# Performance work log

Measured on AMD Instinct MI355X. Metric: run time of the kernel, lower is better.

The kernel has to match this reference:

```python
import jax, jax.numpy as jnp
import numpy as np

B, S, D, H, L, NS = 16, 1024, 512, 8, 4, 4
HD = D // H            # head dim = 64
FF = 4 * D             # dim_feedforward
VOCAB = 64
OUT = 64


def _ln(x, g, b, eps=1e-5):
    m = jnp.mean(x, -1, keepdims=True)
    v = jnp.var(x, -1, keepdims=True)
    return (x - m) * jax.lax.rsqrt(v + eps) * g + b


def setup_inputs() -> dict:
    key = jax.random.key(0)
    ks = iter(jax.random.split(key, 40))
    def w(shape, s=0.02):
        return jax.random.normal(next(ks), shape, jnp.float32) * s
    return {
        "x_batch": jax.random.randint(next(ks), (B, S), 0, VOCAB),
        "context_batch": jax.random.normal(next(ks), (B, 2), jnp.float32),
        "specialist_ids": jax.random.randint(next(ks), (B,), 0, NS),
        "emb_table": w((VOCAB, D), 1.0),
        "wqkv": w((L, D, 3 * D)), "bqkv": jnp.zeros((L, 3 * D), jnp.float32),
        "wo": w((L, D, D)), "bo": jnp.zeros((L, D), jnp.float32),
        "ln1_g": jnp.ones((L, D), jnp.float32), "ln1_b": jnp.zeros((L, D), jnp.float32),
        "w1": w((L, D, FF)), "b1": jnp.zeros((L, FF), jnp.float32),
        "w2": w((L, FF, D)), "b2": jnp.zeros((L, D), jnp.float32),
        "ln2_g": jnp.ones((L, D), jnp.float32), "ln2_b": jnp.zeros((L, D), jnp.float32),
        "ctx_w": w((2, D)), "ctx_b": jnp.zeros((D,), jnp.float32),
        "ca_wq": w((D, D)), "ca_bq": jnp.zeros((D,), jnp.float32),
        "ca_wk": w((D, D)), "ca_bk": jnp.zeros((D,), jnp.float32),
        "ca_wv": w((D, D)), "ca_bv": jnp.zeros((D,), jnp.float32),
        "ca_wo": w((D, D)), "ca_bo": jnp.zeros((D,), jnp.float32),
        "pred_w": w((NS, D, OUT)), "pred_b": jnp.zeros((NS, OUT), jnp.float32),
        "act_w": w((NS, D, OUT)), "act_b": jnp.zeros((NS, OUT), jnp.float32),
    }


def _forward(x_batch, context_batch, specialist_ids, emb_table,
             wqkv, bqkv, wo, bo, ln1_g, ln1_b, w1, b1, w2, b2, ln2_g, ln2_b,
             ctx_w, ctx_b, ca_wq, ca_bq, ca_wk, ca_bk, ca_wv, ca_bv, ca_wo, ca_bo,
             pred_w, pred_b, act_w, act_b):
    b, s = x_batch.shape
    x = emb_table[x_batch]                                   # [B,S,D]
    causal = jnp.triu(jnp.full((s, s), -jnp.inf, jnp.float32), 1)
    scale = 1.0 / np.sqrt(HD)
    nlayers = wqkv.shape[0]
    for i in range(nlayers):  # post-LN TransformerEncoderLayer (torch default)
        qkv = x @ wqkv[i] + bqkv[i]
        q, k, v = jnp.split(qkv, 3, axis=-1)
        q = q.reshape(b, s, H, HD)
        k = k.reshape(b, s, H, HD)
        v = v.reshape(b, s, H, HD)
        scores = jnp.einsum('bqhd,bkhd->bhqk', q, k) * scale + causal
        a = jax.nn.softmax(scores, axis=-1)
        o = jnp.einsum('bhqk,bkhd->bqhd', a, v).reshape(b, s, -1)
        x = _ln(x + o @ wo[i] + bo[i], ln1_g[i], ln1_b[i])
        ff = jax.nn.relu(x @ w1[i] + b1[i]) @ w2[i] + b2[i]
        x = _ln(x + ff, ln2_g[i], ln2_b[i])
    # single-token cross attention: kv comes from projected context
    ctx = (context_batch @ ctx_w + ctx_b)[:, None, :]        # [B,1,D]
    q = (x @ ca_wq + ca_bq).reshape(b, s, H, HD)
    k = (ctx @ ca_wk + ca_bk).reshape(b, 1, H, HD)
    v = (ctx @ ca_wv + ca_bv).reshape(b, 1, H, HD)
    sc = jnp.einsum('bqhd,bkhd->bhqk', q, k) * scale         # [B,H,S,1]
    a = jax.nn.softmax(sc, axis=-1)                          # all ones (kv_len=1)
    o = jnp.einsum('bhqk,bkhd->bqhd', a, v).reshape(b, s, -1)
    latent = o @ ca_wo + ca_bo                               # no residual, as in source
    last = latent[:, -1, :]                                  # [B,D]
    # specialist dispatch: gather per-sample expert weights, batched GEMV
    pred = jnp.einsum('bd,bdo->bo', last, pred_w[specialist_ids]) + pred_b[specialist_ids]
    act = jnp.einsum('bd,bdo->bo', last, act_w[specialist_ids]) + act_b[specialist_ids]
    return pred, act


def reference(x_batch, context_batch, specialist_ids, emb_table,
              wqkv, bqkv, wo, bo, ln1_g, ln1_b, w1, b1, w2, b2, ln2_g, ln2_b,
              ctx_w, ctx_b, ca_wq, ca_bq, ca_wk, ca_bk, ca_wv, ca_bv, ca_wo, ca_bo,
              pred_w, pred_b, act_w, act_b):
    return _forward(x_batch, context_batch, specialist_ids, emb_table,
                    wqkv, bqkv, wo, bo, ln1_g, ln1_b, w1, b1, w2, b2, ln2_g, ln2_b,
                    ctx_w, ctx_b, ca_wq, ca_bq, ca_wk, ca_bk, ca_wv, ca_bv, ca_wo, ca_bo,
                    pred_w, pred_b, act_w, act_b)
```

## Files before the change

kernel.cpp:

```cpp
#include <hip/hip_runtime.h>
#include <hip/hip_bf16.h>


#define DD 512
#define BB 16
#define OO 64
#define NC 8

__global__ __launch_bounds__(256) void k1_v(
    const float* __restrict__ cb, const float* __restrict__ cw,
    const float* __restrict__ cbias, const float* __restrict__ wv,
    float* __restrict__ vpart) {
  __shared__ float cs[BB * 64];
  __shared__ float red[4 * BB * 64];
  const int tid = threadIdx.x;
  const int jb = blockIdx.x & 7, db = blockIdx.x >> 3;
  const int d0 = db * 64, j0 = jb * 64;

  for (int idx = tid; idx < BB * 64; idx += 256) {
    const int b = idx >> 6, d = idx & 63;
    cs[idx] = fmaf(cb[2 * b], cw[d0 + d],
               fmaf(cb[2 * b + 1], cw[DD + d0 + d], cbias[d0 + d]));
  }
  __syncthreads();

  const int j = tid & 63, dsub = tid >> 6;
  float acc[BB];
#pragma unroll
  for (int b = 0; b < BB; ++b) acc[b] = 0.f;
  float wr[16];
#pragma unroll
  for (int i = 0; i < 16; ++i)
    wr[i] = wv[(d0 + dsub * 16 + i) * DD + j0 + j];
#pragma unroll
  for (int i = 0; i < 16; ++i) {
    const int d = dsub * 16 + i;
#pragma unroll
    for (int b = 0; b < BB; ++b) acc[b] = fmaf(cs[b * 64 + d], wr[i], acc[b]);
  }
#pragma unroll
  for (int b = 0; b < BB; ++b) red[dsub * (BB * 64) + b * 64 + j] = acc[b];
  __syncthreads();
  for (int idx = tid; idx < BB * 64; idx += 256) {
    float s = red[idx] + red[idx + BB * 64] + red[idx + 2 * BB * 64] + red[idx + 3 * BB * 64];
    const int b = idx >> 6, jj = idx & 63;
    vpart[(db * BB + b) * DD + j0 + jj] = s;
  }
}

__global__ __launch_bounds__(256) void k2_o(
    const float* __restrict__ bv, const float* __restrict__ wo,
    const float* __restrict__ vpart, float* __restrict__ lpart) {
  __shared__ float vs[BB * 64];
  __shared__ float red[4 * BB * 64];
  const int tid = threadIdx.x;
  const int jb = blockIdx.x & 7, db = blockIdx.x >> 3;
  const int d0 = db * 64, j0 = jb * 64;

  for (int idx = tid; idx < BB * 64; idx += 256) {
    const int b = idx >> 6, d = idx & 63;
    float s = bv[d0 + d];
#pragma unroll
    for (int c = 0; c < NC; ++c) s += vpart[(c * BB + b) * DD + d0 + d];
    vs[idx] = s;
  }
  __syncthreads();

  const int j = tid & 63, dsub = tid >> 6;
  float acc[BB];
#pragma unroll
  for (int b = 0; b < BB; ++b) acc[b] = 0.f;
  float wr[16];
#pragma unroll
  for (int i = 0; i < 16; ++i)
    wr[i] = wo[(d0 + dsub * 16 + i) * DD + j0 + j];
#pragma unroll
  for (int i = 0; i < 16; ++i) {
    const int d = dsub * 16 + i;
#pragma unroll
    for (int b = 0; b < BB; ++b) acc[b] = fmaf(vs[b * 64 + d], wr[i], acc[b]);
  }
#pragma unroll
  for (int b = 0; b < BB; ++b) red[dsub * (BB * 64) + b * 64 + j] = acc[b];
  __syncthreads();
  for (int idx = tid; idx < BB * 64; idx += 256) {
    float s = red[idx] + red[idx + BB * 64] + red[idx + 2 * BB * 64] + red[idx + 3 * BB * 64];
    const int b = idx >> 6, jj = idx & 63;
    lpart[(db * BB + b) * DD + j0 + jj] = s;
  }
}

__global__ __launch_bounds__(512) void k3_head(
    const float* __restrict__ bo, const float* __restrict__ lpart,
    const int* __restrict__ sid,
    const float* __restrict__ pw, const float* __restrict__ pb,
    const float* __restrict__ aw, const float* __restrict__ ab,
    float* __restrict__ out) {
  __shared__ float ls[DD];
  __shared__ float red[8 * OO];
  const int tid = threadIdx.x;
  const int b = blockIdx.x & 15, half = blockIdx.x >> 4;

  for (int d = tid; d < DD; d += 512) {
    float s = bo[d];
#pragma unroll
    for (int c = 0; c < NC; ++c) s += lpart[(c * BB + b) * DD + d];
    ls[d] = s;
  }
  __syncthreads();

  const int s = sid[b];
  const int o = tid & 63, dsub = tid >> 6;
  const float* w = (half ? aw : pw) + (s * DD + dsub * 64) * OO + o;
  float acc = 0.f;
#pragma unroll 16
  for (int i = 0; i < 64; ++i)
    acc = fmaf(ls[dsub * 64 + i], w[i * OO], acc);
  red[dsub * OO + o] = acc;
  __syncthreads();
  if (tid < OO) {
    float a = (half ? ab : pb)[s * OO + tid];
#pragma unroll
    for (int p = 0; p < 8; ++p) a += red[p * OO + tid];
    out[half * (BB * OO) + b * OO + tid] = a;
  }
}

extern "C" void kernel_launch(void* const* d_in, const int* in_sizes, int n_in,
                              void* d_out, int out_size, void* d_ws, size_t ws_size,
                              hipStream_t stream) {
  const float* cb    = reinterpret_cast<const float*>(d_in[1]);
  const int*   sid   = reinterpret_cast<const int*>(d_in[2]);
  const float* cw    = reinterpret_cast<const float*>(d_in[16]);
  const float* cbias = reinterpret_cast<const float*>(d_in[17]);
  const float* wv    = reinterpret_cast<const float*>(d_in[22]);
  const float* bv    = reinterpret_cast<const float*>(d_in[23]);
  const float* wo    = reinterpret_cast<const float*>(d_in[24]);
  const float* bo    = reinterpret_cast<const float*>(d_in[25]);
  const float* pw    = reinterpret_cast<const float*>(d_in[26]);
  const float* pb    = reinterpret_cast<const float*>(d_in[27]);
  const float* aw    = reinterpret_cast<const float*>(d_in[28]);
  const float* ab    = reinterpret_cast<const float*>(d_in[29]);

  float* vpart = reinterpret_cast<float*>(d_ws);
  float* lpart = vpart + NC * BB * DD;

  k1_v   <<<64, 256, 0, stream>>>(cb, cw, cbias, wv, vpart);
  k2_o   <<<64, 256, 0, stream>>>(bv, wo, vpart, lpart);
  k3_head<<<32, 512, 0, stream>>>(bo, lpart, sid, pw, pb, aw, ab,
                                  reinterpret_cast<float*>(d_out));
}
```

Measured before the change: 144.6 us.

## Exploit linearity in context to propagate three basis vectors instead of batch

```diff
diff --git a/kernel.cpp b/kernel.cpp
--- a/kernel.cpp
+++ b/kernel.cpp
@@ -1,5 +1,4 @@
 #include <hip/hip_runtime.h>
-#include <hip/hip_bf16.h>
 
 
 #define DD 512
@@ -7,122 +6,135 @@
 #define OO 64
 #define NC 8
 
-__global__ __launch_bounds__(256) void k1_v(
-    const float* __restrict__ cb, const float* __restrict__ cw,
-    const float* __restrict__ cbias, const float* __restrict__ wv,
-    float* __restrict__ vpart) {
-  __shared__ float cs[BB * 64];
-  __shared__ float red[4 * BB * 64];
+__global__ __launch_bounds__(256) void k1_a(
+    const float* __restrict__ cw, const float* __restrict__ cbias,
+    const float* __restrict__ wv, float* __restrict__ pA) {
+  __shared__ float ts[3 * 64];
+  __shared__ float red[4 * 3 * 64];
   const int tid = threadIdx.x;
   const int jb = blockIdx.x & 7, db = blockIdx.x >> 3;
   const int d0 = db * 64, j0 = jb * 64;
 
-  for (int idx = tid; idx < BB * 64; idx += 256) {
-    const int b = idx >> 6, d = idx & 63;
-    cs[idx] = fmaf(cb[2 * b], cw[d0 + d],
-               fmaf(cb[2 * b + 1], cw[DD + d0 + d], cbias[d0 + d]));
+  if (tid < 192) {
+    const int r = tid >> 6, d = tid & 63;
+    ts[tid] = (r == 0) ? cw[d0 + d] : (r == 1 ? cw[DD + d0 + d] : cbias[d0 + d]);
   }
   __syncthreads();
 
   const int j = tid & 63, dsub = tid >> 6;
-  float acc[BB];
-#pragma unroll
-  for (int b = 0; b < BB; ++b) acc[b] = 0.f;
-  float wr[16];
-#pragma unroll
-  for (int i = 0; i < 16; ++i)
-    wr[i] = wv[(d0 + dsub * 16 + i) * DD + j0 + j];
+  float a0 = 0.f, a1 = 0.f, a2 = 0.f;
 #pragma unroll
   for (int i = 0; i < 16; ++i) {
     const int d = dsub * 16 + i;
-#pragma unroll
-    for (int b = 0; b < BB; ++b) acc[b] = fmaf(cs[b * 64 + d], wr[i], acc[b]);
+    const float w = wv[(d0 + d) * DD + j0 + j];
+    a0 = fmaf(ts[d], w, a0);
+    a1 = fmaf(ts[64 + d], w, a1);
+    a2 = fmaf(ts[128 + d], w, a2);
   }
-#pragma unroll
-  for (int b = 0; b < BB; ++b) red[dsub * (BB * 64) + b * 64 + j] = acc[b];
+  red[(dsub * 3 + 0) * 64 + j] = a0;
+  red[(dsub * 3 + 1) * 64 + j] = a1;
+  red[(dsub * 3 + 2) * 64 + j] = a2;
   __syncthreads();
-  for (int idx = tid; idx < BB * 64; idx += 256) {
-    float s = red[idx] + red[idx + BB * 64] + red[idx + 2 * BB * 64] + red[idx + 3 * BB * 64];
-    const int b = idx >> 6, jj = idx & 63;
-    vpart[(db * BB + b) * DD + j0 + jj] = s;
+  if (tid < 192) {
+    const int r = tid >> 6, jj = tid & 63;
+    pA[(db * 3 + r) * DD + j0 + jj] =
+        red[(0 * 3 + r) * 64 + jj] + red[(1 * 3 + r) * 64 + jj] +
+        red[(2 * 3 + r) * 64 + jj] + red[(3 * 3 + r) * 64 + jj];
   }
 }
 
-__global__ __launch_bounds__(256) void k2_o(
+__global__ __launch_bounds__(256) void k2_b(
     const float* __restrict__ bv, const float* __restrict__ wo,
-    const float* __restrict__ vpart, float* __restrict__ lpart) {
-  __shared__ float vs[BB * 64];
-  __shared__ float red[4 * BB * 64];
+    const float* __restrict__ pA, float* __restrict__ pB) {
+  __shared__ float ts[3 * 64];
+  __shared__ float red[4 * 3 * 64];
   const int tid = threadIdx.x;
   const int jb = blockIdx.x & 7, db = blockIdx.x >> 3;
   const int d0 = db * 64, j0 = jb * 64;
 
-  for (int idx = tid; idx < BB * 64; idx += 256) {
-    const int b = idx >> 6, d = idx & 63;
-    float s = bv[d0 + d];
+  if (tid < 192) {
+    const int r = tid >> 6, d = tid & 63;
+    float s = 0.f;
 #pragma unroll
-    for (int c = 0; c < NC; ++c) s += vpart[(c * BB + b) * DD + d0 + d];
-    vs[idx] = s;
+    for (int c = 0; c < NC; ++c) s += pA[(c * 3 + r) * DD + d0 + d];
+    if (r == 2) s += bv[d0 + d];
+    ts[tid] = s;
   }
   __syncthreads();
 
   const int j = tid & 63, dsub = tid >> 6;
-  float acc[BB];
-#pragma unroll
-  for (int b = 0; b < BB; ++b) acc[b] = 0.f;
-  float wr[16];
-#pragma unroll
-  for (int i = 0; i < 16; ++i)
-    wr[i] = wo[(d0 + dsub * 16 + i) * DD + j0 + j];
+  float a0 = 0.f, a1 = 0.f, a2 = 0.f;
 #pragma unroll
   for (int i = 0; i < 16; ++i) {
     const int d = dsub * 16 + i;
-#pragma unroll
-    for (int b = 0; b < BB; ++b) acc[b] = fmaf(vs[b * 64 + d], wr[i], acc[b]);
+    const float w = wo[(d0 + d) * DD + j0 + j];
+    a0 = fmaf(ts[d], w, a0);
+    a1 = fmaf(ts[64 + d], w, a1);
+    a2 = fmaf(ts[128 + d], w, a2);
   }
-#pragma unroll
-  for (int b = 0; b < BB; ++b) red[dsub * (BB * 64) + b * 64 + j] = acc[b];
+  red[(dsub * 3 + 0) * 64 + j] = a0;
+  red[(dsub * 3 + 1) * 64 + j] = a1;
+  red[(dsub * 3 + 2) * 64 + j] = a2;
   __syncthreads();
-  for (int idx = tid; idx < BB * 64; idx += 256) {
-    float s = red[idx] + red[idx + BB * 64] + red[idx + 2 * BB * 64] + red[idx + 3 * BB * 64];
-    const int b = idx >> 6, jj = idx & 63;
-    lpart[(db * BB + b) * DD + j0 + jj] = s;
+  if (tid < 192) {
+    const int r = tid >> 6, jj = tid & 63;
+    pB[(db * 3 + r) * DD + j0 + jj] =
+        red[(0 * 3 + r) * 64 + jj] + red[(1 * 3 + r) * 64 + jj] +
+        red[(2 * 3 + r) * 64 + jj] + red[(3 * 3 + r) * 64 + jj];
   }
 }
 
 __global__ __launch_bounds__(512) void k3_head(
-    const float* __restrict__ bo, const float* __restrict__ lpart,
-    const int* __restrict__ sid,
+    const float* __restrict__ cb, const int* __restrict__ sid,
+    const float* __restrict__ bo, const float* __restrict__ pB,
     const float* __restrict__ pw, const float* __restrict__ pb,
     const float* __restrict__ aw, const float* __restrict__ ab,
     float* __restrict__ out) {
-  __shared__ float ls[DD];
-  __shared__ float red[8 * OO];
+  __shared__ float Bs[3 * DD];
+  __shared__ float red[8 * 3 * 64];
   const int tid = threadIdx.x;
-  const int b = blockIdx.x & 15, half = blockIdx.x >> 4;
+  const int s = blockIdx.x & 3, half = blockIdx.x >> 2;
 
-  for (int d = tid; d < DD; d += 512) {
-    float s = bo[d];
+  for (int idx = tid; idx < 3 * DD; idx += 512) {
+    const int r = idx >> 9, d = idx & 511;
+    float v = 0.f;
 #pragma unroll
-    for (int c = 0; c < NC; ++c) s += lpart[(c * BB + b) * DD + d];
-    ls[d] = s;
+    for (int c = 0; c < NC; ++c) v += pB[(c * 3 + r) * DD + d];
+    if (r == 2) v += bo[d];
+    Bs[r * DD + d] = v;
   }
   __syncthreads();
 
-  const int s = sid[b];
   const int o = tid & 63, dsub = tid >> 6;
-  const float* w = (half ? aw : pw) + (s * DD + dsub * 64) * OO + o;
-  float acc = 0.f;
+  const float* W = (half ? aw : pw) + s * DD * OO;
+  float a0 = 0.f, a1 = 0.f, a2 = 0.f;
 #pragma unroll 16
-  for (int i = 0; i < 64; ++i)
-    acc = fmaf(ls[dsub * 64 + i], w[i * OO], acc);
-  red[dsub * OO + o] = acc;
+  for (int i = 0; i < 64; ++i) {
+    const int d = dsub * 64 + i;
+    const float w = W[d * OO + o];
+    a0 = fmaf(Bs[d], w, a0);
+    a1 = fmaf(Bs[DD + d], w, a1);
+    a2 = fmaf(Bs[2 * DD + d], w, a2);
+  }
+  red[(dsub * 3 + 0) * 64 + o] = a0;
+  red[(dsub * 3 + 1) * 64 + o] = a1;
+  red[(dsub * 3 + 2) * 64 + o] = a2;
   __syncthreads();
   if (tid < OO) {
-    float a = (half ? ab : pb)[s * OO + tid];
+    float c0 = 0.f, c1 = 0.f, c2 = 0.f;
 #pragma unroll
-    for (int p = 0; p < 8; ++p) a += red[p * OO + tid];
-    out[half * (BB * OO) + b * OO + tid] = a;
+    for (int p = 0; p < 8; ++p) {
+      c0 += red[(p * 3 + 0) * 64 + tid];
+      c1 += red[(p * 3 + 1) * 64 + tid];
+      c2 += red[(p * 3 + 2) * 64 + tid];
+    }
+    const float bias = (half ? ab : pb)[s * OO + tid];
+    for (int b = 0; b < BB; ++b) {
+      if (sid[b] == s) {
+        out[half * (BB * OO) + b * OO + tid] =
+            fmaf(cb[2 * b], c0, fmaf(cb[2 * b + 1], c1, c2 + bias));
+      }
+    }
   }
 }
 
@@ -142,11 +154,11 @@
   const float* aw    = reinterpret_cast<const float*>(d_in[28]);
   const float* ab    = reinterpret_cast<const float*>(d_in[29]);
 
-  float* vpart = reinterpret_cast<float*>(d_ws);
-  float* lpart = vpart + NC * BB * DD;
+  float* pA = reinterpret_cast<float*>(d_ws);
+  float* pB = pA + NC * 3 * DD;
+  float* out = reinterpret_cast<float*>(d_out);
 
-  k1_v   <<<64, 256, 0, stream>>>(cb, cw, cbias, wv, vpart);
-  k2_o   <<<64, 256, 0, stream>>>(bv, wo, vpart, lpart);
-  k3_head<<<32, 512, 0, stream>>>(bo, lpart, sid, pw, pb, aw, ab,
-                                  reinterpret_cast<float*>(d_out));
+  k1_a   <<<64, 256, 0, stream>>>(cw, cbias, wv, pA);
+  k2_b   <<<64, 256, 0, stream>>>(bv, wo, pA, pB);
+  k3_head<<<8, 512, 0, stream>>>(cb, sid, bo, pB, pw, pb, aw, ab, out);
 }
```

After: 143.8 us. Within noise of the previous version (-0.6%).
